# Kernel tuning notes

Measured on AMD Instinct MI355X. Metric: run time of the kernel, lower is better.

## Reference

```python
import jax, jax.numpy as jnp
import numpy as np

N = 100000
MUL = 16


def _build_cg():
    # Real-basis Clebsch-Gordan (Wigner-3j-style) coefficients, shape (2l1+1, 2l2+1, 2lo+1),
    # each normalized to unit Frobenius norm per output component (e3nn component normalization).
    eps = np.zeros((3, 3, 3), np.float32)
    for a, b, c in [(0, 1, 2), (1, 2, 0), (2, 0, 1)]:
        eps[a, b, c] = 1.0
        eps[a, c, b] = -1.0
    s2 = np.float32(1.0 / np.sqrt(2.0))
    q = np.zeros((5, 3, 3), np.float32)  # l=2 real harmonics: xy, yz, 3z^2-r^2, xz, x^2-y^2
    q[0, 0, 1] = q[0, 1, 0] = s2
    q[1, 1, 2] = q[1, 2, 1] = s2
    q[2] = np.diag([-1.0, -1.0, 2.0]).astype(np.float32) / np.sqrt(6.0)
    q[3, 0, 2] = q[3, 2, 0] = s2
    q[4] = np.diag([1.0, -1.0, 0.0]).astype(np.float32) * s2
    cg000 = jnp.ones((1, 1, 1), jnp.float32)                                   # 0e x 0e -> 0e
    cg011 = jnp.asarray(np.eye(3, dtype=np.float32)[None])                      # 0e x 1o -> 1o
    cg110 = jnp.asarray((np.eye(3, dtype=np.float32) / np.sqrt(3.0))[:, :, None])  # 1o x 1o -> 0e
    cg111 = jnp.asarray(eps * s2)                                               # 1o x 1o -> 1e
    cg112 = jnp.asarray(np.transpose(q, (1, 2, 0)))                             # 1o x 1o -> 2e
    return cg000, cg011, cg110, cg111, cg112


def _path(x1, x2, cg, w, alpha):
    # 'uvw' tensor-product path: out[z,w,m] = alpha * sum_{u,v,i,j} x1[z,u,i] x2[z,v,j] cg[i,j,m] w[u,v,w]
    # Contraction order chosen to keep the largest intermediate at [z,u,w,j].
    t = jnp.einsum('zvj,uvw->zuwj', x2, w)
    s = jnp.einsum('zui,zuwj->zwij', x1, t)
    return alpha * jnp.einsum('zwij,ijm->zwm', s, cg)


def _tensor_square(x, w0, w1, w2, w3, w4):
    n = x.shape[0]
    x0 = x[:, :MUL].reshape(n, MUL, 1)       # 16x0e
    x1 = x[:, MUL:].reshape(n, MUL, 3)       # 16x1o
    cg000, cg011, cg110, cg111, cg112 = _build_cg()
    a2 = 1.0 / np.sqrt(MUL * MUL * 2.0)      # 0e output receives 2 paths
    a1 = 1.0 / np.sqrt(MUL * MUL * 1.0)
    o_0e = _path(x0, x0, cg000, w0, a2) + _path(x1, x1, cg110, w2, a2)
    o_1o = _path(x0, x1, cg011, w1, a1)
    o_1e = _path(x1, x1, cg111, w3, a1)
    o_2e = _path(x1, x1, cg112, w4, a1)
    return jnp.concatenate([o.reshape(n, -1) for o in (o_0e, o_1o, o_1e, o_2e)], axis=1)


def setup_inputs() -> dict:
    key = jax.random.key(0)
    kx, k0, k1, k2, k3, k4 = jax.random.split(key, 6)
    return {
        'x': jax.random.normal(kx, (N, MUL * 1 + MUL * 3), jnp.float32),
        'w0': jax.random.normal(k0, (MUL, MUL, MUL), jnp.float32),
        'w1': jax.random.normal(k1, (MUL, MUL, MUL), jnp.float32),
        'w2': jax.random.normal(k2, (MUL, MUL, MUL), jnp.float32),
        'w3': jax.random.normal(k3, (MUL, MUL, MUL), jnp.float32),
        'w4': jax.random.normal(k4, (MUL, MUL, MUL), jnp.float32),
    }


def reference(x, w0, w1, w2, w3, w4):
    return _tensor_square(x, w0, w1, w2, w3, w4)
```

## Files before the change

### kernel.cpp

```cpp
#include <hip/hip_runtime.h>
#include <hip/hip_bf16.h>

typedef __attribute__((ext_vector_type(8))) short short8;
typedef __attribute__((ext_vector_type(4))) float float4v;
typedef __attribute__((ext_vector_type(2))) float float2v;
typedef __attribute__((ext_vector_type(4))) unsigned uint4v;

#define S_A 0.04419417382415922f
#define S_B 0.025515518153991442f
#define S_C 0.0625f

static __device__ __forceinline__ unsigned pkbf(float a, float b) {
#if __has_builtin(__builtin_amdgcn_cvt_pk_bf16_f32)
    auto v = __builtin_amdgcn_cvt_pk_bf16_f32(a, b);
    return __builtin_bit_cast(unsigned, v);
#else
    unsigned ua = __builtin_bit_cast(unsigned, a);
    unsigned ub = __builtin_bit_cast(unsigned, b);
    ua += 0x7fffu + ((ua >> 16) & 1u);
    ub += 0x7fffu + ((ub >> 16) & 1u);
    return __builtin_amdgcn_perm(ub, ua, 0x07060302);
#endif
}

__global__ void wprep_kernel(const float* __restrict__ wA, const float* __restrict__ wB,
                             const float* __restrict__ wC, const float* __restrict__ wD,
                             const float* __restrict__ wE, unsigned short* __restrict__ wout)
{
    int e = blockIdx.x * 256 + threadIdx.x;
    if (e >= 5 * 4096) return;
    int p = e >> 12;
    int rem = e & 4095;
    const float* wp = (p == 0) ? wA : (p == 1) ? wB : (p == 2) ? wC : (p == 3) ? wD : wE;
    unsigned u = __builtin_bit_cast(unsigned, wp[rem]);
    u += 0x7fffu + ((u >> 16) & 1u);
    int k = rem >> 4, w = rem & 15;
    int c = k >> 5, kk = k & 31;
    int lane = ((kk >> 3) << 4) | w;
    int j = kk & 7;
    wout[(((c * 5 + p) * 64 + lane) << 3) | j] = (unsigned short)(u >> 16);
}

template<int G>
static __device__ __forceinline__ void run_group(
    const float* __restrict__ xr, int l, const short8* __restrict__ wbase,
    float* __restrict__ out, long long z0)
{
    const int r  = l & 15;
    const int g  = l >> 4;
    const int v0 = (g & 1) * 8;
    const int uo = g >> 1;

    float2v Xv[4], Yv[4], Zv[4];
    float2v A0v[4];
    {
        float b[24];
        #pragma unroll
        for (int q = 0; q < 6; q++)
            *(float4v*)&b[q * 4] = *(const float4v*)(xr + 16 + v0 * 3 + q * 4);
        #pragma unroll
        for (int t = 0; t < 4; t++) {
            Xv[t] = (float2v){b[6 * t + 0], b[6 * t + 3]};
            Yv[t] = (float2v){b[6 * t + 1], b[6 * t + 4]};
            Zv[t] = (float2v){b[6 * t + 2], b[6 * t + 5]};
        }
        if constexpr (G == 1) {
            float a[8];
            #pragma unroll
            for (int q = 0; q < 2; q++)
                *(float4v*)&a[q * 4] = *(const float4v*)(xr + v0 + q * 4);
            #pragma unroll
            for (int t = 0; t < 4; t++) A0v[t] = (float2v){a[2 * t], a[2 * t + 1]};
        }
    }

    constexpr int NS = (G == 1) ? 4 : 3;
    float4v acc[NS];
    #pragma unroll
    for (int s = 0; s < NS; s++) acc[s] = (float4v){0.f, 0.f, 0.f, 0.f};

    #pragma unroll
    for (int c = 0; c < 8; c++) {
        short8 wfA, wfB, wfC;
        if constexpr (G == 0) wfA = wbase[(c * 5 + 2) * 64 + l];
        if constexpr (G == 1) {
            wfA = wbase[(c * 5 + 0) * 64 + l];
            wfB = wbase[(c * 5 + 1) * 64 + l];
            wfC = wbase[(c * 5 + 4) * 64 + l];
        }
        if constexpr (G == 2) wfA = wbase[(c * 5 + 3) * 64 + l];
        if constexpr (G == 3) wfA = wbase[(c * 5 + 4) * 64 + l];

        const int u = c * 2 + uo;
        float u0 = 0.f, ux = 0.f, uy = 0.f, uz = 0.f;
        if constexpr (G == 0 || G == 1) u0 = xr[u];
        if constexpr (G != 0) {
            ux = xr[16 + u * 3 + 0];
            uy = xr[16 + u * 3 + 1];
            uz = xr[16 + u * 3 + 2];
        }

        unsigned fri[NS][4];
        #pragma unroll
        for (int t = 0; t < 4; t++) {
            const float2v X = Xv[t], Y = Yv[t], Z = Zv[t];
            if constexpr (G == 0) {
                float2v b2 = u0 * X, b3 = u0 * Y, b4 = u0 * Z;
                fri[0][t] = pkbf(b2.x, b2.y);
                fri[1][t] = pkbf(b3.x, b3.y);
                fri[2][t] = pkbf(b4.x, b4.y);
            }
            if constexpr (G == 1) {
                float2v p00 = ux * X, p11 = uy * Y, p22 = uz * Z;
                float2v b0 = u0 * A0v[t];
                float2v b1 = p00 + p11 + p22;
                float2v b10 = 2.0f * p22 - p00 - p11;
                float2v b12 = p00 - p11;
                fri[0][t] = pkbf(b0.x, b0.y);
                fri[1][t] = pkbf(b1.x, b1.y);
                fri[2][t] = pkbf(b10.x, b10.y);
                fri[3][t] = pkbf(b12.x, b12.y);
            }
            if constexpr (G == 2) {
                float2v p01 = ux * Y, p02 = ux * Z, p10 = uy * X;
                float2v p12 = uy * Z, p20 = uz * X, p21 = uz * Y;
                float2v b5 = p12 - p21, b6 = p20 - p02, b7 = p01 - p10;
                fri[0][t] = pkbf(b5.x, b5.y);
                fri[1][t] = pkbf(b6.x, b6.y);
                fri[2][t] = pkbf(b7.x, b7.y);
            }
            if constexpr (G == 3) {
                float2v p01 = ux * Y, p02 = ux * Z, p10 = uy * X;
                float2v p12 = uy * Z, p20 = uz * X, p21 = uz * Y;
                float2v b8 = p01 + p10, b9 = p12 + p21, b11 = p02 + p20;
                fri[0][t] = pkbf(b8.x, b8.y);
                fri[1][t] = pkbf(b9.x, b9.y);
                fri[2][t] = pkbf(b11.x, b11.y);
            }
        }

        #pragma unroll
        for (int s = 0; s < NS; s++) {
            short8 frm = __builtin_bit_cast(short8, *(uint4v*)fri[s]);
            const short8& wf = (G == 1) ? ((s == 0) ? wfA : (s == 1) ? wfB : wfC) : wfA;
            acc[s] = __builtin_amdgcn_mfma_f32_16x16x32_bf16(frm, wf, acc[s], 0, 0, 0);
        }
    }

    const int w = r;
    float* outp = out + (z0 + g * 4) * 192;
    #pragma unroll
    for (int reg = 0; reg < 4; reg++) {
        float* rowp = outp + reg * 192;
        if constexpr (G == 0) {
            rowp[16 + w * 3 + 0] = S_C * acc[0][reg];
            rowp[16 + w * 3 + 1] = S_C * acc[1][reg];
            rowp[16 + w * 3 + 2] = S_C * acc[2][reg];
        }
        if constexpr (G == 1) {
            rowp[w]               = S_A * acc[0][reg] + S_B * acc[1][reg];
            rowp[112 + w * 5 + 2] = S_B * acc[2][reg];
            rowp[112 + w * 5 + 4] = S_A * acc[3][reg];
        }
        if constexpr (G == 2) {
            rowp[64 + w * 3 + 0] = S_A * acc[0][reg];
            rowp[64 + w * 3 + 1] = S_A * acc[1][reg];
            rowp[64 + w * 3 + 2] = S_A * acc[2][reg];
        }
        if constexpr (G == 3) {
            rowp[112 + w * 5 + 0] = S_A * acc[0][reg];
            rowp[112 + w * 5 + 1] = S_A * acc[1][reg];
            rowp[112 + w * 5 + 3] = S_A * acc[2][reg];
        }
    }
}

__global__ __launch_bounds__(256)
void tsq_kernel(const float* __restrict__ x,
                const unsigned short* __restrict__ wfrag,
                float* __restrict__ out,
                int nrows)
{
    __shared__ __attribute__((aligned(16))) float xlds[16 * 68];

    const int tid = threadIdx.x;
    const long long z0 = (long long)blockIdx.x * 16;

    {
        const float* xg = x + z0 * 64;
        int f = tid * 4;
        int row = f >> 6, col = f & 63;
        float4v v = {0.f, 0.f, 0.f, 0.f};
        if (z0 + row < nrows) v = *(const float4v*)(xg + f);
        *(float4v*)&xlds[row * 68 + col] = v;
    }
    __syncthreads();
    if (z0 >= nrows) return;

    const int wave = tid >> 6;
    const int l = tid & 63;
    const float* xr = &xlds[(l & 15) * 68];
    const short8* wbase = (const short8*)wfrag;

    if      (wave == 0) run_group<0>(xr, l, wbase, out, z0);
    else if (wave == 1) run_group<1>(xr, l, wbase, out, z0);
    else if (wave == 2) run_group<2>(xr, l, wbase, out, z0);
    else                run_group<3>(xr, l, wbase, out, z0);
}

extern "C" void kernel_launch(void* const* d_in, const int* in_sizes, int n_in,
                              void* d_out, int out_size, void* d_ws, size_t ws_size,
                              hipStream_t stream) {
    const float* x  = (const float*)d_in[0];
    const float* w0 = (const float*)d_in[1];
    const float* w1 = (const float*)d_in[2];
    const float* w2 = (const float*)d_in[3];
    const float* w3 = (const float*)d_in[4];
    const float* w4 = (const float*)d_in[5];
    float* out = (float*)d_out;
    unsigned short* wfrag = (unsigned short*)d_ws;
    (void)ws_size; (void)n_in; (void)out_size;

    const int nrows = in_sizes[0] / 64;
    const int nblocks = (nrows + 15) / 16;

    wprep_kernel<<<dim3(80), dim3(256), 0, stream>>>(w0, w2, w1, w3, w4, wfrag);
    tsq_kernel<<<dim3(nblocks), dim3(256), 0, stream>>>(x, wfrag, out, nrows);
}
```

Measured before the change: 134.7 us.

## Rebalance MFMA path work across three waves and prefetch weight fragments

Redistributes the 13 bilinear feature streams from four waves per block (4/3/3/3 MFMAs) to three waves (4/5/4), so each block uses 192 threads and the x tile load is split into two passes. It also software-pipelines the weight fragment global loads by fetching chunk c+1 while computing chunk c, and shares products such as p01/p02/p12 between symmetric and antisymmetric combinations. The goal is less per-block wave overhead, hidden weight-load latency, and fewer redundant multiplies, at the cost of more VGPRs and a longer critical path per wave.

New measurement: 137.6 us. +2.2%, slower.

```diff
diff --git a/kernel.cpp b/kernel.cpp
--- a/kernel.cpp
+++ b/kernel.cpp
@@ -42,6 +42,13 @@
 }
 
 template<int G>
+static __device__ __forceinline__ int pathof(int i) {
+    if constexpr (G == 0) return (i == 0) ? 0 : (i == 1) ? 1 : 4;
+    if constexpr (G == 1) return (i == 0) ? 2 : (i == 1) ? 3 : 4;
+    return (i == 0) ? 3 : 4;
+}
+
+template<int G>
 static __device__ __forceinline__ void run_group(
     const float* __restrict__ xr, int l, const short8* __restrict__ wbase,
     float* __restrict__ out, long long z0)
@@ -64,7 +71,7 @@
             Yv[t] = (float2v){b[6 * t + 1], b[6 * t + 4]};
             Zv[t] = (float2v){b[6 * t + 2], b[6 * t + 5]};
         }
-        if constexpr (G == 1) {
+        if constexpr (G == 0) {
             float a[8];
             #pragma unroll
             for (int q = 0; q < 2; q++)
@@ -74,77 +81,84 @@
         }
     }
 
-    constexpr int NS = (G == 1) ? 4 : 3;
+    constexpr int NS = (G == 1) ? 5 : 4;
+    constexpr int NP = (G == 2) ? 2 : 3;
+
     float4v acc[NS];
     #pragma unroll
     for (int s = 0; s < NS; s++) acc[s] = (float4v){0.f, 0.f, 0.f, 0.f};
 
+    short8 wcur[NP], wnxt[NP];
+    #pragma unroll
+    for (int i = 0; i < NP; i++) wcur[i] = wbase[(0 * 5 + pathof<G>(i)) * 64 + l];
+
     #pragma unroll
     for (int c = 0; c < 8; c++) {
-        short8 wfA, wfB, wfC;
-        if constexpr (G == 0) wfA = wbase[(c * 5 + 2) * 64 + l];
-        if constexpr (G == 1) {
-            wfA = wbase[(c * 5 + 0) * 64 + l];
-            wfB = wbase[(c * 5 + 1) * 64 + l];
-            wfC = wbase[(c * 5 + 4) * 64 + l];
-        }
-        if constexpr (G == 2) wfA = wbase[(c * 5 + 3) * 64 + l];
-        if constexpr (G == 3) wfA = wbase[(c * 5 + 4) * 64 + l];
+        if (c < 7) {
+            #pragma unroll
+            for (int i = 0; i < NP; i++) wnxt[i] = wbase[((c + 1) * 5 + pathof<G>(i)) * 64 + l];
+        }
 
         const int u = c * 2 + uo;
-        float u0 = 0.f, ux = 0.f, uy = 0.f, uz = 0.f;
-        if constexpr (G == 0 || G == 1) u0 = xr[u];
-        if constexpr (G != 0) {
-            ux = xr[16 + u * 3 + 0];
-            uy = xr[16 + u * 3 + 1];
-            uz = xr[16 + u * 3 + 2];
-        }
+        float u0 = 0.f, ux = 0.f, uy, uz;
+        if constexpr (G != 2) u0 = xr[u];
+        if constexpr (G != 1) ux = xr[16 + u * 3 + 0];
+        uy = xr[16 + u * 3 + 1];
+        uz = xr[16 + u * 3 + 2];
 
         unsigned fri[NS][4];
         #pragma unroll
         for (int t = 0; t < 4; t++) {
             const float2v X = Xv[t], Y = Yv[t], Z = Zv[t];
             if constexpr (G == 0) {
-                float2v b2 = u0 * X, b3 = u0 * Y, b4 = u0 * Z;
-                fri[0][t] = pkbf(b2.x, b2.y);
-                fri[1][t] = pkbf(b3.x, b3.y);
-                fri[2][t] = pkbf(b4.x, b4.y);
-            }
-            if constexpr (G == 1) {
+                float2v b0  = u0 * A0v[t];
                 float2v p00 = ux * X, p11 = uy * Y, p22 = uz * Z;
-                float2v b0 = u0 * A0v[t];
-                float2v b1 = p00 + p11 + p22;
-                float2v b10 = 2.0f * p22 - p00 - p11;
+                float2v t01 = p00 + p11;
+                float2v b1  = t01 + p22;
+                float2v b10 = 2.0f * p22 - t01;
                 float2v b12 = p00 - p11;
                 fri[0][t] = pkbf(b0.x, b0.y);
                 fri[1][t] = pkbf(b1.x, b1.y);
                 fri[2][t] = pkbf(b10.x, b10.y);
                 fri[3][t] = pkbf(b12.x, b12.y);
             }
+            if constexpr (G == 1) {
+                float2v b2 = u0 * X, b3 = u0 * Y, b4 = u0 * Z;
+                float2v p12 = uy * Z;
+                float2v b5 = p12 - uz * Y;
+                float2v b9 = p12 + uz * Y;
+                fri[0][t] = pkbf(b2.x, b2.y);
+                fri[1][t] = pkbf(b3.x, b3.y);
+                fri[2][t] = pkbf(b4.x, b4.y);
+                fri[3][t] = pkbf(b5.x, b5.y);
+                fri[4][t] = pkbf(b9.x, b9.y);
+            }
             if constexpr (G == 2) {
-                float2v p01 = ux * Y, p02 = ux * Z, p10 = uy * X;
-                float2v p12 = uy * Z, p20 = uz * X, p21 = uz * Y;
-                float2v b5 = p12 - p21, b6 = p20 - p02, b7 = p01 - p10;
-                fri[0][t] = pkbf(b5.x, b5.y);
-                fri[1][t] = pkbf(b6.x, b6.y);
-                fri[2][t] = pkbf(b7.x, b7.y);
-            }
-            if constexpr (G == 3) {
-                float2v p01 = ux * Y, p02 = ux * Z, p10 = uy * X;
-                float2v p12 = uy * Z, p20 = uz * X, p21 = uz * Y;
-                float2v b8 = p01 + p10, b9 = p12 + p21, b11 = p02 + p20;
-                fri[0][t] = pkbf(b8.x, b8.y);
-                fri[1][t] = pkbf(b9.x, b9.y);
-                fri[2][t] = pkbf(b11.x, b11.y);
+                float2v p01 = ux * Y;
+                float2v b7  = p01 - uy * X;
+                float2v b8  = p01 + uy * X;
+                float2v p02 = ux * Z;
+                float2v b6  = uz * X - p02;
+                float2v b11 = p02 + uz * X;
+                fri[0][t] = pkbf(b6.x, b6.y);
+                fri[1][t] = pkbf(b7.x, b7.y);
+                fri[2][t] = pkbf(b8.x, b8.y);
+                fri[3][t] = pkbf(b11.x, b11.y);
             }
         }
 
         #pragma unroll
         for (int s = 0; s < NS; s++) {
             short8 frm = __builtin_bit_cast(short8, *(uint4v*)fri[s]);
-            const short8& wf = (G == 1) ? ((s == 0) ? wfA : (s == 1) ? wfB : wfC) : wfA;
-            acc[s] = __builtin_amdgcn_mfma_f32_16x16x32_bf16(frm, wf, acc[s], 0, 0, 0);
-        }
+            int wi;
+            if constexpr (G == 0) wi = (s == 0) ? 0 : (s == 1) ? 1 : 2;
+            if constexpr (G == 1) wi = (s <= 2) ? 0 : (s == 3) ? 1 : 2;
+            if constexpr (G == 2) wi = (s <= 1) ? 0 : 1;
+            acc[s] = __builtin_amdgcn_mfma_f32_16x16x32_bf16(frm, wcur[wi], acc[s], 0, 0, 0);
+        }
+
+        #pragma unroll
+        for (int i = 0; i < NP; i++) wcur[i] = wnxt[i];
     }
 
     const int w = r;
@@ -153,29 +167,27 @@
     for (int reg = 0; reg < 4; reg++) {
         float* rowp = outp + reg * 192;
         if constexpr (G == 0) {
-            rowp[16 + w * 3 + 0] = S_C * acc[0][reg];
-            rowp[16 + w * 3 + 1] = S_C * acc[1][reg];
-            rowp[16 + w * 3 + 2] = S_C * acc[2][reg];
-        }
-        if constexpr (G == 1) {
             rowp[w]               = S_A * acc[0][reg] + S_B * acc[1][reg];
             rowp[112 + w * 5 + 2] = S_B * acc[2][reg];
             rowp[112 + w * 5 + 4] = S_A * acc[3][reg];
         }
+        if constexpr (G == 1) {
+            rowp[16 + w * 3 + 0]  = S_C * acc[0][reg];
+            rowp[16 + w * 3 + 1]  = S_C * acc[1][reg];
+            rowp[16 + w * 3 + 2]  = S_C * acc[2][reg];
+            rowp[64 + w * 3 + 0]  = S_A * acc[3][reg];
+            rowp[112 + w * 5 + 1] = S_A * acc[4][reg];
+        }
         if constexpr (G == 2) {
-            rowp[64 + w * 3 + 0] = S_A * acc[0][reg];
-            rowp[64 + w * 3 + 1] = S_A * acc[1][reg];
-            rowp[64 + w * 3 + 2] = S_A * acc[2][reg];
-        }
-        if constexpr (G == 3) {
-            rowp[112 + w * 5 + 0] = S_A * acc[0][reg];
-            rowp[112 + w * 5 + 1] = S_A * acc[1][reg];
-            rowp[112 + w * 5 + 3] = S_A * acc[2][reg];
-        }
-    }
-}
-
-__global__ __launch_bounds__(256)
+            rowp[64 + w * 3 + 1]  = S_A * acc[0][reg];
+            rowp[64 + w * 3 + 2]  = S_A * acc[1][reg];
+            rowp[112 + w * 5 + 0] = S_A * acc[2][reg];
+            rowp[112 + w * 5 + 3] = S_A * acc[3][reg];
+        }
+    }
+}
+
+__global__ __launch_bounds__(192, 4)
 void tsq_kernel(const float* __restrict__ x,
                 const unsigned short* __restrict__ wfrag,
                 float* __restrict__ out,
@@ -188,11 +200,20 @@
 
     {
         const float* xg = x + z0 * 64;
-        int f = tid * 4;
-        int row = f >> 6, col = f & 63;
-        float4v v = {0.f, 0.f, 0.f, 0.f};
-        if (z0 + row < nrows) v = *(const float4v*)(xg + f);
-        *(float4v*)&xlds[row * 68 + col] = v;
+        {
+            int f = tid * 4;
+            int row = f >> 6, col = f & 63;
+            float4v v = {0.f, 0.f, 0.f, 0.f};
+            if (z0 + row < nrows) v = *(const float4v*)(xg + f);
+            *(float4v*)&xlds[row * 68 + col] = v;
+        }
+        if (tid < 64) {
+            int f = 768 + tid * 4;
+            int row = f >> 6, col = f & 63;
+            float4v v = {0.f, 0.f, 0.f, 0.f};
+            if (z0 + row < nrows) v = *(const float4v*)(xg + f);
+            *(float4v*)&xlds[row * 68 + col] = v;
+        }
     }
     __syncthreads();
     if (z0 >= nrows) return;
@@ -204,8 +225,7 @@
 
     if      (wave == 0) run_group<0>(xr, l, wbase, out, z0);
     else if (wave == 1) run_group<1>(xr, l, wbase, out, z0);
-    else if (wave == 2) run_group<2>(xr, l, wbase, out, z0);
-    else                run_group<3>(xr, l, wbase, out, z0);
+    else                run_group<2>(xr, l, wbase, out, z0);
 }
 
 extern "C" void kernel_launch(void* const* d_in, const int* in_sizes, int n_in,
@@ -225,5 +245,5 @@
     const int nblocks = (nrows + 15) / 16;
 
     wprep_kernel<<<dim3(80), dim3(256), 0, stream>>>(w0, w2, w1, w3, w4, wfrag);
-    tsq_kernel<<<dim3(nblocks), dim3(256), 0, stream>>>(x, wfrag, out, nrows);
-}
+    tsq_kernel<<<dim3(nblocks), dim3(192), 0, stream>>>(x, wfrag, out, nrows);
+}
```
